# Performance work log

Measured on AMD Instinct MI355X. Metric: run time of the kernel, lower is better.

Reference implementation:

```python
import jax, jax.numpy as jnp
import numpy as np

N = 50000
E = 800000
DIN = 64   # input_dim
DE = 32    # edge_dim
HID = 32   # hidden_dim (per-head channels for layers 0,1)
DOUT = 64  # output_dim


def _lin_init(key, fan_in, fan_out):
    return jax.random.normal(key, (fan_in, fan_out), dtype=jnp.float32) / np.sqrt(fan_in)


def setup_inputs() -> dict:
    key = jax.random.key(0)
    ks = list(jax.random.split(key, 64))
    inp = {}
    inp["x"] = jax.random.normal(ks[0], (N, DIN), dtype=jnp.float32)
    inp["edge_attr"] = jax.random.normal(ks[1], (E, DE), dtype=jnp.float32)
    inp["edge_index"] = jax.random.randint(ks[2], (2, E), 0, N, dtype=jnp.int32)
    # layer dims: (in_dim, heads, per-head out C, skip_out)
    dims = [(DIN, 2, HID, 2 * HID), (2 * HID, 2, HID, 2 * HID), (2 * HID, 1, DOUT, DOUT)]
    ki = 3
    for l, (din, H, C, dskip) in enumerate(dims):
        HC = H * C
        inp[f"Wq{l}"] = _lin_init(ks[ki], din, HC); ki += 1
        inp[f"bq{l}"] = jnp.zeros((HC,), jnp.float32)
        inp[f"Wk{l}"] = _lin_init(ks[ki], din, HC); ki += 1
        inp[f"bk{l}"] = jnp.zeros((HC,), jnp.float32)
        inp[f"Wv{l}"] = _lin_init(ks[ki], din, HC); ki += 1
        inp[f"bv{l}"] = jnp.zeros((HC,), jnp.float32)
        inp[f"We{l}"] = _lin_init(ks[ki], DE, HC); ki += 1  # lin_edge, bias=False in PyG
        inp[f"Ws{l}"] = _lin_init(ks[ki], din, dskip); ki += 1  # lin_skip (root weight)
        inp[f"bs{l}"] = jnp.zeros((dskip,), jnp.float32)
    inp["prelu_a"] = jnp.asarray(0.25, dtype=jnp.float32)
    return inp


def _transformer_conv(x, src, dst, eattr, Wq, bq, Wk, bk, Wv, bv, We, Ws, bs, H, C, concat):
    n = x.shape[0]
    q = (x @ Wq + bq).reshape(n, H, C)
    k = (x @ Wk + bk).reshape(n, H, C)
    v = (x @ Wv + bv).reshape(n, H, C)
    e = (eattr @ We).reshape(-1, H, C)          # [E,H,C] edge embedding
    kj = k[src] + e                              # key of source + edge
    alpha = jnp.sum(q[dst] * kj, axis=-1) / jnp.sqrt(jnp.float32(C))  # [E,H]
    # scatter softmax over incoming edges per destination node
    m = jax.ops.segment_max(alpha, dst, num_segments=n)
    a = jnp.exp(alpha - m[dst])
    s = jax.ops.segment_sum(a, dst, num_segments=n)
    a = a / (s[dst] + 1e-16)
    vj = v[src] + e                              # value of source + edge
    out = jax.ops.segment_sum(a[..., None] * vj, dst, num_segments=n)  # [N,H,C]
    out = out.reshape(n, H * C) if concat else jnp.mean(out, axis=1)
    return out + x @ Ws + bs                     # root/skip connection


def reference(x, edge_attr, edge_index,
              Wq0, bq0, Wk0, bk0, Wv0, bv0, We0, Ws0, bs0,
              Wq1, bq1, Wk1, bk1, Wv1, bv1, We1, Ws1, bs1,
              Wq2, bq2, Wk2, bk2, Wv2, bv2, We2, Ws2, bs2,
              prelu_a):
    src, dst = edge_index[0], edge_index[1]
    h = _transformer_conv(x, src, dst, edge_attr, Wq0, bq0, Wk0, bk0, Wv0, bv0, We0, Ws0, bs0, 2, HID, True)
    h = jnp.where(h >= 0, h, prelu_a * h)
    h = _transformer_conv(h, src, dst, edge_attr, Wq1, bq1, Wk1, bk1, Wv1, bv1, We1, Ws1, bs1, 2, HID, True)
    h = jnp.where(h >= 0, h, prelu_a * h)
    h = _transformer_conv(h, src, dst, edge_attr, Wq2, bq2, Wk2, bk2, Wv2, bv2, We2, Ws2, bs2, 1, DOUT, False)
    return h
```

## Files before the change

kernel.cpp:

```cpp
#include <hip/hip_runtime.h>
#include <hip/hip_bf16.h>


#define NDIM 64

static __device__ __forceinline__ float b2f(__hip_bfloat16 v) { return __bfloat162float(v); }
static __device__ __forceinline__ unsigned short f2bu(float f) {
  __hip_bfloat16 b = __float2bfloat16(f);
  return *reinterpret_cast<unsigned short*>(&b);
}

__global__ void k_count(const int* __restrict__ ei, int* __restrict__ cnt, int E) {
  int i = blockIdx.x * blockDim.x + threadIdx.x;
  if (i < E) atomicAdd(&cnt[ei[E + i]], 1);
}

__global__ __launch_bounds__(256) void k_scanA(const int* __restrict__ cnt,
                                               int* __restrict__ tpre,
                                               int* __restrict__ btot, int n) {
  int t = threadIdx.x, b = blockIdx.x;
  int base = (b * 256 + t) * 4;
  int s = 0;
  if (base + 3 < n) {
    int4 v = *(const int4*)(cnt + base);
    s = v.x + v.y + v.z + v.w;
  } else if (base < n) {
    for (int k = 0; k < 4 && base + k < n; ++k) s += cnt[base + k];
  }
  __shared__ int ps[256];
  ps[t] = s;
  __syncthreads();
  for (int off = 1; off < 256; off <<= 1) {
    int v = (t >= off) ? ps[t - off] : 0;
    __syncthreads();
    ps[t] += v;
    __syncthreads();
  }
  tpre[b * 256 + t] = ps[t] - s;
  if (t == 255) btot[b] = ps[255];
}

__global__ void k_scanB(int* __restrict__ btot, int nb, int* __restrict__ rowptr, int n) {
  int lane = threadIdx.x & 63;
  int v = (lane < nb) ? btot[lane] : 0;
  int inc = v;
#pragma unroll
  for (int off = 1; off < 64; off <<= 1) {
    int u = __shfl_up(inc, off);
    if (lane >= off) inc += u;
  }
  if (lane < nb) btot[lane] = inc - v;
  if (lane == 63) rowptr[n] = inc;
}

__global__ __launch_bounds__(256) void k_scanC(const int* __restrict__ cnt,
                                               const int* __restrict__ tpre,
                                               const int* __restrict__ btot,
                                               int* __restrict__ rowptr, int n) {
  int t = threadIdx.x, b = blockIdx.x;
  int base = (b * 256 + t) * 4;
  if (base >= n) return;
  int p = btot[b] + tpre[b * 256 + t];
  if (base + 3 < n) {
    int4 v = *(const int4*)(cnt + base);
    rowptr[base] = p; p += v.x;
    rowptr[base + 1] = p; p += v.y;
    rowptr[base + 2] = p; p += v.z;
    rowptr[base + 3] = p;
  } else {
    for (int k = 0; k < 4 && base + k < n; ++k) { rowptr[base + k] = p; p += cnt[base + k]; }
  }
}

__global__ void k_scatter(const int* __restrict__ ei, int* __restrict__ fill,
                          const int* __restrict__ rowptr,
                          const float4* __restrict__ ea,
                          int* __restrict__ srcs, ushort4* __restrict__ eab, int E) {
  int i = blockIdx.x * blockDim.x + threadIdx.x;
  if (i < E) {
    int d = ei[E + i];
    int pos = rowptr[d] + atomicAdd(&fill[d], 1);
    srcs[pos] = ei[i];
    const float4* s = ea + (size_t)i * 8;
    ushort4* o = eab + (size_t)pos * 8;
#pragma unroll
    for (int j = 0; j < 8; ++j) {
      float4 v = s[j];
      ushort4 u;
      u.x = f2bu(v.x); u.y = f2bu(v.y); u.z = f2bu(v.z); u.w = f2bu(v.w);
      o[j] = u;
    }
  }
}

__global__ __launch_bounds__(256) void k_node(
    const float* __restrict__ h,
    const float* __restrict__ Wq, const float* __restrict__ bq,
    const float* __restrict__ Wk, const float* __restrict__ bk,
    const float* __restrict__ Wv, const float* __restrict__ bv,
    const float* __restrict__ Ws, const float* __restrict__ bs,
    float* __restrict__ qs, __hip_bfloat16* __restrict__ kvb, int N)
{
  __shared__ float hL[64][64];
  int t = threadIdx.x;
  int nb = blockIdx.x * 64;
  int m = t >> 6, c = t & 63;
  const float* W = (m == 0) ? Wq : (m == 1) ? Wk : (m == 2) ? Wv : Ws;
  const float* B = (m == 0) ? bq : (m == 1) ? bk : (m == 2) ? bv : bs;
  float w[64];
#pragma unroll
  for (int d = 0; d < 64; ++d) w[d] = W[d * 64 + c];
  float bias = B[c];
  int nmax = N - nb; if (nmax > 64) nmax = 64;
#pragma unroll
  for (int j = 0; j < 16; ++j) {
    int flat = j * 256 + t;
    int ni = flat >> 6;
    if (ni < nmax) hL[ni][flat & 63] = h[(size_t)(nb + ni) * 64 + (flat & 63)];
  }
  __syncthreads();
  for (int i = 0; i < nmax; ++i) {
    float acc = bias;
    const float4* hr = (const float4*)&hL[i][0];
#pragma unroll
    for (int d4 = 0; d4 < 16; ++d4) {
      float4 hv = hr[d4];
      acc = fmaf(hv.x, w[4 * d4 + 0], acc);
      acc = fmaf(hv.y, w[4 * d4 + 1], acc);
      acc = fmaf(hv.z, w[4 * d4 + 2], acc);
      acc = fmaf(hv.w, w[4 * d4 + 3], acc);
    }
    size_t n = (size_t)(nb + i);
    if (m == 0)      qs[n * 128 + c] = acc;
    else if (m == 3) qs[n * 128 + 64 + c] = acc;
    else             kvb[n * 128 + ((m == 2) ? 64 : 0) + c] = __float2bfloat16(acc);
  }
}

template <int H>
__global__ __launch_bounds__(256) void k_qe(const float* __restrict__ qs,
                                            const float* __restrict__ We,
                                            float* __restrict__ qe, int N)
{
  __shared__ float WeT[64][32];
  int t = threadIdx.x;
#pragma unroll
  for (int f = t; f < 2048; f += 256) WeT[f >> 5][f & 31] = We[(f & 31) * 64 + (f >> 5)];
  __syncthreads();
  int gid = blockIdx.x * 256 + t;
  if (gid >= N * 64) return;
  int n = gid >> 6, slot = gid & 63;
  if (H == 1 && slot >= 32) { qe[gid] = 0.f; return; }
  float acc = 0.f;
  if (H == 2) {
    int hh = slot >> 5, d = slot & 31;
    const float* qrow = qs + (size_t)n * 128 + hh * 32;
#pragma unroll
    for (int c = 0; c < 32; ++c) acc = fmaf(qrow[c], WeT[hh * 32 + c][d], acc);
  } else {
    int d = slot;
    const float* qrow = qs + (size_t)n * 128;
#pragma unroll
    for (int c = 0; c < 64; ++c) acc = fmaf(qrow[c], WeT[c][d], acc);
  }
  qe[gid] = acc;
}

template <int H, bool LAST>
__global__ __launch_bounds__(256) void k_attn(
    const float* __restrict__ qs,
    const __hip_bfloat16* __restrict__ kvb,
    const float* __restrict__ qe,
    const __hip_bfloat16* __restrict__ eab,
    const float* __restrict__ We,
    const int* __restrict__ rowptr,
    const int* __restrict__ srcs,
    const float* __restrict__ prelu_a,
    float* __restrict__ hout, int N)
{
  int wave = threadIdx.x >> 6;
  int lane = threadIdx.x & 63;
  int dst = blockIdx.x * 4 + wave;
  if (dst >= N) return;
  const float rsC = (H == 2) ? 0.17677669529663687f : 0.125f;
  const int RW = (H == 2) ? 32 : 64;
  int el = lane & 31;

  float q_c = qs[(size_t)dst * 128 + lane];
  float qe_c = qe[(size_t)dst * 64 + lane];

  float m = -1e30f, s = 0.f, accv = 0.f, acce = 0.f;
  int jb = rowptr[dst], je = rowptr[dst + 1];
  int j = jb;
  for (; j + 4 <= je; j += 4) {
    int s0 = srcs[j], s1 = srcs[j + 1], s2 = srcs[j + 2], s3 = srcs[j + 3];
    const __hip_bfloat16* r0 = kvb + (size_t)s0 * 128;
    const __hip_bfloat16* r1 = kvb + (size_t)s1 * 128;
    const __hip_bfloat16* r2 = kvb + (size_t)s2 * 128;
    const __hip_bfloat16* r3 = kvb + (size_t)s3 * 128;
    float k0 = b2f(r0[lane]), v0 = b2f(r0[64 + lane]);
    float k1 = b2f(r1[lane]), v1 = b2f(r1[64 + lane]);
    float k2 = b2f(r2[lane]), v2 = b2f(r2[64 + lane]);
    float k3 = b2f(r3[lane]), v3 = b2f(r3[64 + lane]);
    float a0 = b2f(eab[(size_t)(j + 0) * 32 + el]);
    float a1 = b2f(eab[(size_t)(j + 1) * 32 + el]);
    float a2 = b2f(eab[(size_t)(j + 2) * 32 + el]);
    float a3 = b2f(eab[(size_t)(j + 3) * 32 + el]);
    float x0 = fmaf(q_c, k0, qe_c * a0);
    float x1 = fmaf(q_c, k1, qe_c * a1);
    float x2 = fmaf(q_c, k2, qe_c * a2);
    float x3 = fmaf(q_c, k3, qe_c * a3);
#pragma unroll
    for (int off = 1; off < RW; off <<= 1) {
      x0 += __shfl_xor(x0, off);
      x1 += __shfl_xor(x1, off);
      x2 += __shfl_xor(x2, off);
      x3 += __shfl_xor(x3, off);
    }
    x0 *= rsC; x1 *= rsC; x2 *= rsC; x3 *= rsC;
    float mx = fmaxf(fmaxf(x0, x1), fmaxf(x2, x3));
    float mn = fmaxf(m, mx);
    float sc = __expf(m - mn);
    float q0 = __expf(x0 - mn), q1 = __expf(x1 - mn);
    float q2 = __expf(x2 - mn), q3 = __expf(x3 - mn);
    s = s * sc + ((q0 + q1) + (q2 + q3));
    accv = accv * sc + (fmaf(q0, v0, q1 * v1) + fmaf(q2, v2, q3 * v3));
    acce = acce * sc + (fmaf(q0, a0, q1 * a1) + fmaf(q2, a2, q3 * a3));
    m = mn;
  }
  for (; j < je; ++j) {
    int s0 = srcs[j];
    const __hip_bfloat16* r0 = kvb + (size_t)s0 * 128;
    float k0 = b2f(r0[lane]), v0 = b2f(r0[64 + lane]);
    float a0 = b2f(eab[(size_t)j * 32 + el]);
    float x0 = fmaf(q_c, k0, qe_c * a0);
#pragma unroll
    for (int off = 1; off < RW; off <<= 1) x0 += __shfl_xor(x0, off);
    x0 *= rsC;
    float mn = fmaxf(m, x0);
    float sc = __expf(m - mn);
    float q0 = __expf(x0 - mn);
    s = s * sc + q0;
    accv = accv * sc + q0 * v0;
    acce = acce * sc + q0 * a0;
    m = mn;
  }

  float wecol[32];
#pragma unroll
  for (int d = 0; d < 32; ++d) wecol[d] = We[d * 64 + lane];
  int base = (H == 2) ? (lane & 32) : 0;
  float sum = accv;
#pragma unroll
  for (int d = 0; d < 32; ++d) {
    float aead = __shfl(acce, base + d);
    sum = fmaf(aead, wecol[d], sum);
  }
  float out = sum / (s + 1e-16f);
  out += qs[(size_t)dst * 128 + 64 + lane];
  if (!LAST) {
    float a = prelu_a[0];
    out = (out >= 0.f) ? out : a * out;
  }
  hout[(size_t)dst * 64 + lane] = out;
}

extern "C" void kernel_launch(void* const* d_in, const int* in_sizes, int n_in,
                              void* d_out, int out_size, void* d_ws, size_t ws_size,
                              hipStream_t stream) {
  const int N = in_sizes[0] / NDIM;
  const int E = in_sizes[2] / 2;

  const float* x  = (const float*)d_in[0];
  const float* ea = (const float*)d_in[1];
  const int* ei   = (const int*)d_in[2];
  const float* prelu = (const float*)d_in[30];
  auto W = [&](int l, int k) { return (const float*)d_in[3 + 9 * l + k]; };

  const int nbScan = (N + 1023) / 1024;

  char* p = (char*)d_ws;
  auto alloc = [&](size_t bytes) { char* r = p; p += (bytes + 255) & ~(size_t)255; return r; };
  float* h             = (float*)alloc((size_t)N * 64 * 4);
  float* qs            = (float*)alloc((size_t)N * 128 * 4);
  __hip_bfloat16* kvb  = (__hip_bfloat16*)alloc((size_t)N * 128 * 2);
  float* qe            = (float*)alloc((size_t)N * 64 * 4);
  __hip_bfloat16* eab  = (__hip_bfloat16*)alloc((size_t)E * 32 * 2);
  int* rowptr          = (int*)alloc((size_t)(N + 1) * 4);
  int* cnt             = (int*)alloc((size_t)N * 4);
  int* fill            = (int*)alloc((size_t)N * 4);
  int* srcs            = (int*)alloc((size_t)E * 4);
  int* tpre            = (int*)alloc((size_t)nbScan * 256 * 4);
  int* btot            = (int*)alloc((size_t)64 * 4);
  (void)ws_size; (void)n_in; (void)out_size;

  hipMemsetAsync(cnt, 0, (size_t)N * 4, stream);
  hipMemsetAsync(fill, 0, (size_t)N * 4, stream);

  k_count<<<(E + 255) / 256, 256, 0, stream>>>(ei, cnt, E);
  k_scanA<<<nbScan, 256, 0, stream>>>(cnt, tpre, btot, N);
  k_scanB<<<1, 64, 0, stream>>>(btot, nbScan, rowptr, N);
  k_scanC<<<nbScan, 256, 0, stream>>>(cnt, tpre, btot, rowptr, N);
  k_scatter<<<(E + 255) / 256, 256, 0, stream>>>(ei, fill, rowptr, (const float4*)ea,
                                                 srcs, (ushort4*)eab, E);

  for (int l = 0; l < 3; ++l) {
    const float* hin = (l == 0) ? x : h;
    k_node<<<(N + 63) / 64, 256, 0, stream>>>(
        hin, W(l, 0), W(l, 1), W(l, 2), W(l, 3), W(l, 4), W(l, 5), W(l, 7), W(l, 8), qs, kvb, N);
    if (l < 2) {
      k_qe<2><<<(N * 64 + 255) / 256, 256, 0, stream>>>(qs, W(l, 6), qe, N);
      k_attn<2, false><<<(N + 3) / 4, 256, 0, stream>>>(
          qs, kvb, qe, eab, W(l, 6), rowptr, srcs, prelu, h, N);
    } else {
      k_qe<1><<<(N * 64 + 255) / 256, 256, 0, stream>>>(qs, W(l, 6), qe, N);
      k_attn<1, true><<<(N + 3) / 4, 256, 0, stream>>>(
          qs, kvb, qe, eab, W(l, 6), rowptr, srcs, prelu, (float*)d_out, N);
    }
  }
}
```

Before: 814.4 us.

## Fuse qe into node kernel, interleave k/v, lazy softmax rescale, persistent attn waves

Several changes land together. The q·We projection moves into k_node via shared memory, which removes the k_qe launch and its reread of qs. K and V are interleaved into one 32-bit word per lane so each source row needs a single gather, and the edge-attribute permutation moves to a separate coalesced kernel driven by a perm array. The attention kernel now uses exp2 with the scale and log2e folded into q, rescales the online softmax only when the running max grows by more than 16, and has each wave handle four destinations so the We column load is amortised. The two memsets are merged into one. The lazy rescale adds a data-dependent branch and relies on exp2 staying in range.

```diff
diff --git a/kernel.cpp b/kernel.cpp
--- a/kernel.cpp
+++ b/kernel.cpp
@@ -3,8 +3,8 @@
 
 
 #define NDIM 64
-
-static __device__ __forceinline__ float b2f(__hip_bfloat16 v) { return __bfloat162float(v); }
+#define LOG2E 1.4426950408889634f
+
 static __device__ __forceinline__ unsigned short f2bu(float f) {
   __hip_bfloat16 b = __float2bfloat16(f);
   return *reinterpret_cast<unsigned short*>(&b);
@@ -74,34 +74,43 @@
 
 __global__ void k_scatter(const int* __restrict__ ei, int* __restrict__ fill,
                           const int* __restrict__ rowptr,
-                          const float4* __restrict__ ea,
-                          int* __restrict__ srcs, ushort4* __restrict__ eab, int E) {
+                          int* __restrict__ srcs, int* __restrict__ perm, int E) {
   int i = blockIdx.x * blockDim.x + threadIdx.x;
   if (i < E) {
     int d = ei[E + i];
     int pos = rowptr[d] + atomicAdd(&fill[d], 1);
     srcs[pos] = ei[i];
-    const float4* s = ea + (size_t)i * 8;
-    ushort4* o = eab + (size_t)pos * 8;
-#pragma unroll
-    for (int j = 0; j < 8; ++j) {
-      float4 v = s[j];
-      ushort4 u;
-      u.x = f2bu(v.x); u.y = f2bu(v.y); u.z = f2bu(v.z); u.w = f2bu(v.w);
-      o[j] = u;
-    }
-  }
-}
-
+    perm[pos] = i;
+  }
+}
+
+__global__ __launch_bounds__(256) void k_permea(const int* __restrict__ perm,
+                                                const float4* __restrict__ ea,
+                                                ushort4* __restrict__ eab, int E) {
+  int tid = blockIdx.x * 256 + threadIdx.x;
+  int pos = tid >> 3, t = tid & 7;
+  if (pos >= E) return;
+  int i = perm[pos];
+  float4 v = ea[(size_t)i * 8 + t];
+  ushort4 u;
+  u.x = f2bu(v.x); u.y = f2bu(v.y); u.z = f2bu(v.z); u.w = f2bu(v.w);
+  eab[(size_t)pos * 8 + t] = u;
+}
+
+template <int H>
 __global__ __launch_bounds__(256) void k_node(
     const float* __restrict__ h,
     const float* __restrict__ Wq, const float* __restrict__ bq,
     const float* __restrict__ Wk, const float* __restrict__ bk,
     const float* __restrict__ Wv, const float* __restrict__ bv,
     const float* __restrict__ Ws, const float* __restrict__ bs,
-    float* __restrict__ qs, __hip_bfloat16* __restrict__ kvb, int N)
+    const float* __restrict__ We,
+    float* __restrict__ qs, unsigned int* __restrict__ kvw,
+    float* __restrict__ qe, int N)
 {
   __shared__ float hL[64][64];
+  __shared__ float qL[64][64];
+  __shared__ float WeT[2048];
   int t = threadIdx.x;
   int nb = blockIdx.x * 64;
   int m = t >> 6, c = t & 63;
@@ -111,6 +120,8 @@
 #pragma unroll
   for (int d = 0; d < 64; ++d) w[d] = W[d * 64 + c];
   float bias = B[c];
+#pragma unroll
+  for (int f = t; f < 2048; f += 256) WeT[(f >> 5) * 32 + (f & 31)] = We[(f & 31) * 64 + (f >> 5)];
   int nmax = N - nb; if (nmax > 64) nmax = 64;
 #pragma unroll
   for (int j = 0; j < 16; ++j) {
@@ -131,45 +142,43 @@
       acc = fmaf(hv.w, w[4 * d4 + 3], acc);
     }
     size_t n = (size_t)(nb + i);
-    if (m == 0)      qs[n * 128 + c] = acc;
+    if (m == 0)      { qs[n * 128 + c] = acc; qL[i][c] = acc; }
     else if (m == 3) qs[n * 128 + 64 + c] = acc;
-    else             kvb[n * 128 + ((m == 2) ? 64 : 0) + c] = __float2bfloat16(acc);
-  }
-}
-
-template <int H>
-__global__ __launch_bounds__(256) void k_qe(const float* __restrict__ qs,
-                                            const float* __restrict__ We,
-                                            float* __restrict__ qe, int N)
-{
-  __shared__ float WeT[64][32];
-  int t = threadIdx.x;
-#pragma unroll
-  for (int f = t; f < 2048; f += 256) WeT[f >> 5][f & 31] = We[(f & 31) * 64 + (f >> 5)];
+    else ((unsigned short*)kvw)[(n * 64 + c) * 2 + (m == 2 ? 1 : 0)] = f2bu(acc);
+  }
   __syncthreads();
-  int gid = blockIdx.x * 256 + t;
-  if (gid >= N * 64) return;
-  int n = gid >> 6, slot = gid & 63;
-  if (H == 1 && slot >= 32) { qe[gid] = 0.f; return; }
-  float acc = 0.f;
-  if (H == 2) {
-    int hh = slot >> 5, d = slot & 31;
-    const float* qrow = qs + (size_t)n * 128 + hh * 32;
-#pragma unroll
-    for (int c = 0; c < 32; ++c) acc = fmaf(qrow[c], WeT[hh * 32 + c][d], acc);
-  } else {
-    int d = slot;
-    const float* qrow = qs + (size_t)n * 128;
-#pragma unroll
-    for (int c = 0; c < 64; ++c) acc = fmaf(qrow[c], WeT[c][d], acc);
-  }
-  qe[gid] = acc;
+  int slot = t & 63, ibase = (t >> 6) * 16;
+  int half = slot >> 5, d = slot & 31;
+  float wreg[32];
+#pragma unroll
+  for (int cc = 0; cc < 32; ++cc) wreg[cc] = WeT[(half * 32 + cc) * 32 + d];
+  for (int ii = 0; ii < 16; ++ii) {
+    int i = ibase + ii;
+    if (i >= nmax) break;
+    float acc = 0.f;
+    const float4* qr = (const float4*)&qL[i][half * 32];
+#pragma unroll
+    for (int c4 = 0; c4 < 8; ++c4) {
+      float4 qv = qr[c4];
+      acc = fmaf(qv.x, wreg[4 * c4 + 0], acc);
+      acc = fmaf(qv.y, wreg[4 * c4 + 1], acc);
+      acc = fmaf(qv.z, wreg[4 * c4 + 2], acc);
+      acc = fmaf(qv.w, wreg[4 * c4 + 3], acc);
+    }
+    size_t n = (size_t)(nb + i);
+    if (H == 2) {
+      qe[n * 64 + slot] = acc;
+    } else {
+      float tot = acc + __shfl_xor(acc, 32);
+      qe[n * 64 + slot] = (slot < 32) ? tot : 0.f;
+    }
+  }
 }
 
 template <int H, bool LAST>
 __global__ __launch_bounds__(256) void k_attn(
     const float* __restrict__ qs,
-    const __hip_bfloat16* __restrict__ kvb,
+    const unsigned int* __restrict__ kvw,
     const float* __restrict__ qe,
     const __hip_bfloat16* __restrict__ eab,
     const float* __restrict__ We,
@@ -180,89 +189,94 @@
 {
   int wave = threadIdx.x >> 6;
   int lane = threadIdx.x & 63;
-  int dst = blockIdx.x * 4 + wave;
-  if (dst >= N) return;
-  const float rsC = (H == 2) ? 0.17677669529663687f : 0.125f;
+  int wgid = blockIdx.x * 4 + wave;
+  const int W = gridDim.x * 4;
+  const float pmul = ((H == 2) ? 0.17677669529663687f : 0.125f) * LOG2E;
   const int RW = (H == 2) ? 32 : 64;
   int el = lane & 31;
 
-  float q_c = qs[(size_t)dst * 128 + lane];
-  float qe_c = qe[(size_t)dst * 64 + lane];
-
-  float m = -1e30f, s = 0.f, accv = 0.f, acce = 0.f;
-  int jb = rowptr[dst], je = rowptr[dst + 1];
-  int j = jb;
-  for (; j + 4 <= je; j += 4) {
-    int s0 = srcs[j], s1 = srcs[j + 1], s2 = srcs[j + 2], s3 = srcs[j + 3];
-    const __hip_bfloat16* r0 = kvb + (size_t)s0 * 128;
-    const __hip_bfloat16* r1 = kvb + (size_t)s1 * 128;
-    const __hip_bfloat16* r2 = kvb + (size_t)s2 * 128;
-    const __hip_bfloat16* r3 = kvb + (size_t)s3 * 128;
-    float k0 = b2f(r0[lane]), v0 = b2f(r0[64 + lane]);
-    float k1 = b2f(r1[lane]), v1 = b2f(r1[64 + lane]);
-    float k2 = b2f(r2[lane]), v2 = b2f(r2[64 + lane]);
-    float k3 = b2f(r3[lane]), v3 = b2f(r3[64 + lane]);
-    float a0 = b2f(eab[(size_t)(j + 0) * 32 + el]);
-    float a1 = b2f(eab[(size_t)(j + 1) * 32 + el]);
-    float a2 = b2f(eab[(size_t)(j + 2) * 32 + el]);
-    float a3 = b2f(eab[(size_t)(j + 3) * 32 + el]);
-    float x0 = fmaf(q_c, k0, qe_c * a0);
-    float x1 = fmaf(q_c, k1, qe_c * a1);
-    float x2 = fmaf(q_c, k2, qe_c * a2);
-    float x3 = fmaf(q_c, k3, qe_c * a3);
-#pragma unroll
-    for (int off = 1; off < RW; off <<= 1) {
-      x0 += __shfl_xor(x0, off);
-      x1 += __shfl_xor(x1, off);
-      x2 += __shfl_xor(x2, off);
-      x3 += __shfl_xor(x3, off);
-    }
-    x0 *= rsC; x1 *= rsC; x2 *= rsC; x3 *= rsC;
-    float mx = fmaxf(fmaxf(x0, x1), fmaxf(x2, x3));
-    float mn = fmaxf(m, mx);
-    float sc = __expf(m - mn);
-    float q0 = __expf(x0 - mn), q1 = __expf(x1 - mn);
-    float q2 = __expf(x2 - mn), q3 = __expf(x3 - mn);
-    s = s * sc + ((q0 + q1) + (q2 + q3));
-    accv = accv * sc + (fmaf(q0, v0, q1 * v1) + fmaf(q2, v2, q3 * v3));
-    acce = acce * sc + (fmaf(q0, a0, q1 * a1) + fmaf(q2, a2, q3 * a3));
-    m = mn;
-  }
-  for (; j < je; ++j) {
-    int s0 = srcs[j];
-    const __hip_bfloat16* r0 = kvb + (size_t)s0 * 128;
-    float k0 = b2f(r0[lane]), v0 = b2f(r0[64 + lane]);
-    float a0 = b2f(eab[(size_t)j * 32 + el]);
-    float x0 = fmaf(q_c, k0, qe_c * a0);
-#pragma unroll
-    for (int off = 1; off < RW; off <<= 1) x0 += __shfl_xor(x0, off);
-    x0 *= rsC;
-    float mn = fmaxf(m, x0);
-    float sc = __expf(m - mn);
-    float q0 = __expf(x0 - mn);
-    s = s * sc + q0;
-    accv = accv * sc + q0 * v0;
-    acce = acce * sc + q0 * a0;
-    m = mn;
-  }
-
   float wecol[32];
 #pragma unroll
   for (int d = 0; d < 32; ++d) wecol[d] = We[d * 64 + lane];
-  int base = (H == 2) ? (lane & 32) : 0;
-  float sum = accv;
-#pragma unroll
-  for (int d = 0; d < 32; ++d) {
-    float aead = __shfl(acce, base + d);
-    sum = fmaf(aead, wecol[d], sum);
-  }
-  float out = sum / (s + 1e-16f);
-  out += qs[(size_t)dst * 128 + 64 + lane];
-  if (!LAST) {
-    float a = prelu_a[0];
-    out = (out >= 0.f) ? out : a * out;
-  }
-  hout[(size_t)dst * 64 + lane] = out;
+  float pa = LAST ? 0.f : prelu_a[0];
+
+  for (int rep = 0; rep < 4; ++rep) {
+    int dst = wgid + rep * W;
+    if (dst >= N) break;
+
+    float q_c = qs[(size_t)dst * 128 + lane] * pmul;
+    float qe_c = qe[(size_t)dst * 64 + lane] * pmul;
+
+    float m = -1e30f, s = 0.f, accv = 0.f, acce = 0.f;
+    int jb = rowptr[dst], je = rowptr[dst + 1];
+    int j = jb;
+    for (; j + 4 <= je; j += 4) {
+      int s0 = srcs[j], s1 = srcs[j + 1], s2 = srcs[j + 2], s3 = srcs[j + 3];
+      unsigned int w0 = kvw[(size_t)s0 * 64 + lane];
+      unsigned int w1 = kvw[(size_t)s1 * 64 + lane];
+      unsigned int w2 = kvw[(size_t)s2 * 64 + lane];
+      unsigned int w3 = kvw[(size_t)s3 * 64 + lane];
+      float a0 = __uint_as_float(((unsigned int)*(const unsigned short*)&eab[(size_t)(j + 0) * 32 + el]) << 16);
+      float a1 = __uint_as_float(((unsigned int)*(const unsigned short*)&eab[(size_t)(j + 1) * 32 + el]) << 16);
+      float a2 = __uint_as_float(((unsigned int)*(const unsigned short*)&eab[(size_t)(j + 2) * 32 + el]) << 16);
+      float a3 = __uint_as_float(((unsigned int)*(const unsigned short*)&eab[(size_t)(j + 3) * 32 + el]) << 16);
+      float k0 = __uint_as_float(w0 << 16), v0 = __uint_as_float(w0 & 0xFFFF0000u);
+      float k1 = __uint_as_float(w1 << 16), v1 = __uint_as_float(w1 & 0xFFFF0000u);
+      float k2 = __uint_as_float(w2 << 16), v2 = __uint_as_float(w2 & 0xFFFF0000u);
+      float k3 = __uint_as_float(w3 << 16), v3 = __uint_as_float(w3 & 0xFFFF0000u);
+      float x0 = fmaf(q_c, k0, qe_c * a0);
+      float x1 = fmaf(q_c, k1, qe_c * a1);
+      float x2 = fmaf(q_c, k2, qe_c * a2);
+      float x3 = fmaf(q_c, k3, qe_c * a3);
+#pragma unroll
+      for (int off = 1; off < RW; off <<= 1) {
+        x0 += __shfl_xor(x0, off);
+        x1 += __shfl_xor(x1, off);
+        x2 += __shfl_xor(x2, off);
+        x3 += __shfl_xor(x3, off);
+      }
+      float mx = fmaxf(fmaxf(x0, x1), fmaxf(x2, x3));
+      if (__any(mx > m + 16.f)) {
+        float mn = fmaxf(m, mx);
+        float sc = exp2f(m - mn);
+        s *= sc; accv *= sc; acce *= sc;
+        m = mn;
+      }
+      float q0 = exp2f(x0 - m), q1 = exp2f(x1 - m);
+      float q2 = exp2f(x2 - m), q3 = exp2f(x3 - m);
+      s += (q0 + q1) + (q2 + q3);
+      accv += fmaf(q0, v0, q1 * v1) + fmaf(q2, v2, q3 * v3);
+      acce += fmaf(q0, a0, q1 * a1) + fmaf(q2, a2, q3 * a3);
+    }
+    for (; j < je; ++j) {
+      int s0 = srcs[j];
+      unsigned int w0 = kvw[(size_t)s0 * 64 + lane];
+      float k0 = __uint_as_float(w0 << 16), v0 = __uint_as_float(w0 & 0xFFFF0000u);
+      float a0 = __uint_as_float(((unsigned int)*(const unsigned short*)&eab[(size_t)j * 32 + el]) << 16);
+      float x0 = fmaf(q_c, k0, qe_c * a0);
+#pragma unroll
+      for (int off = 1; off < RW; off <<= 1) x0 += __shfl_xor(x0, off);
+      float mn = fmaxf(m, x0);
+      float sc = exp2f(m - mn);
+      float q0 = exp2f(x0 - mn);
+      s = s * sc + q0;
+      accv = accv * sc + q0 * v0;
+      acce = acce * sc + q0 * a0;
+      m = mn;
+    }
+
+    int base = (H == 2) ? (lane & 32) : 0;
+    float sum = accv;
+#pragma unroll
+    for (int d = 0; d < 32; ++d) {
+      float aead = __shfl(acce, base + d);
+      sum = fmaf(aead, wecol[d], sum);
+    }
+    float out = sum / (s + 1e-16f);
+    out += qs[(size_t)dst * 128 + 64 + lane];
+    if (!LAST) out = (out >= 0.f) ? out : pa * out;
+    hout[(size_t)dst * 64 + lane] = out;
+  }
 }
 
 extern "C" void kernel_launch(void* const* d_in, const int* in_sizes, int n_in,
@@ -283,39 +297,43 @@
   auto alloc = [&](size_t bytes) { char* r = p; p += (bytes + 255) & ~(size_t)255; return r; };
   float* h             = (float*)alloc((size_t)N * 64 * 4);
   float* qs            = (float*)alloc((size_t)N * 128 * 4);
-  __hip_bfloat16* kvb  = (__hip_bfloat16*)alloc((size_t)N * 128 * 2);
+  unsigned int* kvw    = (unsigned int*)alloc((size_t)N * 64 * 4);
   float* qe            = (float*)alloc((size_t)N * 64 * 4);
   __hip_bfloat16* eab  = (__hip_bfloat16*)alloc((size_t)E * 32 * 2);
   int* rowptr          = (int*)alloc((size_t)(N + 1) * 4);
-  int* cnt             = (int*)alloc((size_t)N * 4);
-  int* fill            = (int*)alloc((size_t)N * 4);
+  int* cntfill         = (int*)alloc((size_t)2 * N * 4);
+  int* cnt = cntfill;
+  int* fill = cntfill + N;
   int* srcs            = (int*)alloc((size_t)E * 4);
+  int* perm            = (int*)alloc((size_t)E * 4);
   int* tpre            = (int*)alloc((size_t)nbScan * 256 * 4);
   int* btot            = (int*)alloc((size_t)64 * 4);
   (void)ws_size; (void)n_in; (void)out_size;
 
-  hipMemsetAsync(cnt, 0, (size_t)N * 4, stream);
-  hipMemsetAsync(fill, 0, (size_t)N * 4, stream);
+  hipMemsetAsync(cntfill, 0, (size_t)2 * N * 4, stream);
 
   k_count<<<(E + 255) / 256, 256, 0, stream>>>(ei, cnt, E);
   k_scanA<<<nbScan, 256, 0, stream>>>(cnt, tpre, btot, N);
   k_scanB<<<1, 64, 0, stream>>>(btot, nbScan, rowptr, N);
   k_scanC<<<nbScan, 256, 0, stream>>>(cnt, tpre, btot, rowptr, N);
-  k_scatter<<<(E + 255) / 256, 256, 0, stream>>>(ei, fill, rowptr, (const float4*)ea,
-                                                 srcs, (ushort4*)eab, E);
-
+  k_scatter<<<(E + 255) / 256, 256, 0, stream>>>(ei, fill, rowptr, srcs, perm, E);
+  k_permea<<<(E * 8 + 255) / 256, 256, 0, stream>>>(perm, (const float4*)ea, (ushort4*)eab, E);
+
+  const int attnBlocks = (N + 15) / 16;
   for (int l = 0; l < 3; ++l) {
     const float* hin = (l == 0) ? x : h;
-    k_node<<<(N + 63) / 64, 256, 0, stream>>>(
-        hin, W(l, 0), W(l, 1), W(l, 2), W(l, 3), W(l, 4), W(l, 5), W(l, 7), W(l, 8), qs, kvb, N);
     if (l < 2) {
-      k_qe<2><<<(N * 64 + 255) / 256, 256, 0, stream>>>(qs, W(l, 6), qe, N);
-      k_attn<2, false><<<(N + 3) / 4, 256, 0, stream>>>(
-          qs, kvb, qe, eab, W(l, 6), rowptr, srcs, prelu, h, N);
+      k_node<2><<<(N + 63) / 64, 256, 0, stream>>>(
+          hin, W(l, 0), W(l, 1), W(l, 2), W(l, 3), W(l, 4), W(l, 5), W(l, 7), W(l, 8),
+          W(l, 6), qs, kvw, qe, N);
+      k_attn<2, false><<<attnBlocks, 256, 0, stream>>>(
+          qs, kvw, qe, eab, W(l, 6), rowptr, srcs, prelu, h, N);
     } else {
-      k_qe<1><<<(N * 64 + 255) / 256, 256, 0, stream>>>(qs, W(l, 6), qe, N);
-      k_attn<1, true><<<(N + 3) / 4, 256, 0, stream>>>(
-          qs, kvb, qe, eab, W(l, 6), rowptr, srcs, prelu, (float*)d_out, N);
-    }
-  }
-}
+      k_node<1><<<(N + 63) / 64, 256, 0, stream>>>(
+          hin, W(l, 0), W(l, 1), W(l, 2), W(l, 3), W(l, 4), W(l, 5), W(l, 7), W(l, 8),
+          W(l, 6), qs, kvw, qe, N);
+      k_attn<1, true><<<attnBlocks, 256, 0, stream>>>(
+          qs, kvw, qe, eab, W(l, 6), rowptr, srcs, prelu, (float*)d_out, N);
+    }
+  }
+}
```

Measured after the change: 784.2 us. 1.04x faster.
